# Kernel optimization log

Measured on AMD Instinct MI355X. Metric: run time of the kernel, lower is better.

Reference implementation:

```python
import jax, jax.numpy as jnp
import numpy as np

N, C, E = 50000, 128, 400000
R_CUT = 5.0


def setup_inputs() -> dict:
    key = jax.random.key(0)
    ks = jax.random.split(key, 12)
    s = jax.random.normal(ks[0], (N, C), dtype=jnp.float32)
    v = jax.random.normal(ks[1], (N, 3, C), dtype=jnp.float32)
    edges = jax.random.randint(ks[2], (E, 2), 0, N, dtype=jnp.int64)
    r_ij = jax.random.uniform(ks[3], (E, 1), dtype=jnp.float32, minval=0.1, maxval=R_CUT)
    rn = jax.random.normal(ks[4], (E, 3), dtype=jnp.float32)
    r_ij_normalized = rn / jnp.linalg.norm(rn, axis=-1, keepdims=True)
    sc = 1.0 / np.sqrt(C)
    W1 = jax.random.normal(ks[5], (C, C), dtype=jnp.float32) * sc
    b1 = jnp.zeros((C,), dtype=jnp.float32)
    W2 = jax.random.normal(ks[6], (C, 3 * C), dtype=jnp.float32) * sc
    b2 = jnp.zeros((3 * C,), dtype=jnp.float32)
    Wr = jax.random.normal(ks[7], (20, 3 * C), dtype=jnp.float32) * (1.0 / np.sqrt(20))
    br = jnp.zeros((3 * C,), dtype=jnp.float32)
    return {"s": s, "v": v, "edges": edges, "r_ij": r_ij,
            "r_ij_normalized": r_ij_normalized,
            "W1": W1, "b1": b1, "W2": W2, "b2": b2, "Wr": Wr, "br": br}


def rbf(r_ij, r_cut):
    # r_ij: [E,1] -> [E,20]; sin(n*pi/r_cut * r) / r for n=1..20
    n = jnp.arange(1, 21, dtype=r_ij.dtype)  # [20]
    return jnp.sin((np.pi / r_cut) * n * r_ij) / r_ij


def fcut(r_ij, r_cut):
    return 0.5 * (jnp.cos(np.pi * r_ij / r_cut) + 1.0)  # [E,1]


def reference(s, v, edges, r_ij, r_ij_normalized, W1, b1, W2, b2, Wr, br):
    r_cut = R_CUT
    src = edges[:, 1]
    dst = edges[:, 0]
    # RBF filter: [E,3C], modulated by cosine cutoff
    rbf_pass = (rbf(r_ij, r_cut) @ Wr + br) * fcut(r_ij, r_cut)
    # node MLP: Linear -> SiLU -> Linear : [N,3C]
    s_pass = jax.nn.silu(s @ W1 + b1) @ W2 + b2
    pass_out = rbf_pass * s_pass[src]  # [E,3C]
    dv, ds, drep = jnp.split(pass_out, 3, axis=-1)  # each [E,C]
    # [E,3,C] = gathered v * gate + direction * rep
    delta_v = v[src] * dv[:, None, :] + r_ij_normalized[:, :, None] * drep[:, None, :]
    s_out = s + jax.ops.segment_sum(ds, dst, num_segments=N)
    v_out = v + jax.ops.segment_sum(delta_v, dst, num_segments=N)
    return s_out, v_out
```

## Files before the change

### kernel.cpp

```cpp
#include <hip/hip_runtime.h>
#include <hip/hip_bf16.h>

#define CC 128
#define NOUT 384
#define PI_F 3.14159265358979323846f
#define RCUT 5.0f

typedef float f32x2 __attribute__((ext_vector_type(2)));
typedef __attribute__((ext_vector_type(8))) short bf16x8;
typedef __attribute__((ext_vector_type(4))) float f32x4;

__device__ __forceinline__ float loadF(const void* p, size_t i, int isf32) {
  if (isf32) return ((const float*)p)[i];
  unsigned int w = ((unsigned int)((const unsigned short*)p)[i]) << 16;
  return __uint_as_float(w);
}
__device__ __forceinline__ int loadI(const void* p, size_t i, int isi64) {
  if (isi64) return (int)((const long long*)p)[i];
  return ((const int*)p)[i];
}
__device__ __forceinline__ unsigned int bfbits(float f) {
  __hip_bfloat16 h = __float2bfloat16(f);
  unsigned short u;
  __builtin_memcpy(&u, &h, 2);
  return (unsigned int)u;
}
__device__ __forceinline__ unsigned int bfpack(float lo, float hi) {
  return bfbits(lo) | (bfbits(hi) << 16);
}
__device__ __forceinline__ float bf16lo(unsigned int u) {
  return __uint_as_float(u << 16);
}
__device__ __forceinline__ float bf16hi(unsigned int u) {
  return __uint_as_float(u & 0xffff0000u);
}

__global__ void detect_kernel(const void* s, const void* edges, int* flags) {
  if (threadIdx.x == 0) {
    int isf32 = 0;
    const unsigned short* us = (const unsigned short*)s;
    for (int i = 0; i < 1024; i++) {
      unsigned int w = ((unsigned int)us[i]) << 16;
      float f = __uint_as_float(w);
      if (!(fabsf(f) < 1000.f)) { isf32 = 1; break; }
    }
    int isi64 = 1;
    const int* ie = (const int*)edges;
    for (int i = 1; i < 128; i += 2) {
      if (ie[i] != 0) { isi64 = 0; break; }
    }
    flags[0] = isf32;
    flags[1] = isi64;
  }
}

__global__ void count_kernel(const void* __restrict__ edges, int* __restrict__ cnt,
                             const int* __restrict__ flags, int E) {
  int e = blockIdx.x * blockDim.x + threadIdx.x;
  if (e >= E) return;
  int dst = loadI(edges, (size_t)2 * e, flags[1]);
  atomicAdd(&cnt[dst], 1);
}

__global__ __launch_bounds__(1024) void scan_kernel(const int* __restrict__ cnt,
                                                    int* __restrict__ row_start,
                                                    int* __restrict__ next, int N) {
  __shared__ int woff[16];
  __shared__ int carry_sh;
  const int t = threadIdx.x;
  const int lane = t & 63;
  const int wid = t >> 6;
  if (t == 0) carry_sh = 0;
  __syncthreads();
  for (int base = 0; base < N; base += 1024) {
    int x = (base + t < N) ? cnt[base + t] : 0;
    int incl = x;
    #pragma unroll
    for (int off = 1; off < 64; off <<= 1) {
      int y = __shfl_up(incl, off, 64);
      if (lane >= off) incl += y;
    }
    if (lane == 63) woff[wid] = incl;
    __syncthreads();
    if (wid == 0 && lane < 16) {
      int w = woff[lane];
      int iw = w;
      #pragma unroll
      for (int off = 1; off < 16; off <<= 1) {
        int y = __shfl_up(iw, off, 64);
        if (lane >= off) iw += y;
      }
      woff[lane] = iw - w;
    }
    __syncthreads();
    int carry = carry_sh;
    int excl = carry + woff[wid] + incl - x;
    if (base + t < N) { row_start[base + t] = excl; next[base + t] = excl; }
    __syncthreads();
    if (t == 1023) carry_sh = excl + x;
    __syncthreads();
  }
  if (t == 0) row_start[N] = carry_sh;
}

template <int PRE>
__global__ void fill_kernel(const void* __restrict__ edges,
                            const void* __restrict__ r_ij,
                            const void* __restrict__ rn,
                            int* __restrict__ next,
                            int* __restrict__ esrc,
                            float4* __restrict__ efcrn,
                            float* __restrict__ erb,
                            const int* __restrict__ flags, int E) {
  int e = blockIdx.x * blockDim.x + threadIdx.x;
  if (e >= E) return;
  const int isi64 = flags[1];
  const int isf32 = flags[0];
  const int dst = loadI(edges, (size_t)2 * e, isi64);
  const int src = loadI(edges, (size_t)2 * e + 1, isi64);
  const float r  = loadF(r_ij, e, isf32);
  const float r0 = loadF(rn, (size_t)e * 3 + 0, isf32);
  const float r1 = loadF(rn, (size_t)e * 3 + 1, isf32);
  const float r2 = loadF(rn, (size_t)e * 3 + 2, isf32);
  const int p = atomicAdd(&next[dst], 1);
  esrc[p] = src;
  if (PRE) {
    const float x = (PI_F / RCUT) * r;
    const float s1 = __sinf(x);
    const float c1 = __cosf(x);
    const float fc = 0.5f * (c1 + 1.f);
    efcrn[p] = make_float4(fc, r0, r1, r2);
    const float rf = __builtin_amdgcn_rcpf(r) * fc;
    const float twoc = 2.f * c1;
    float sp = 0.f, sn = s1;
    float rbv[20];
    #pragma unroll
    for (int k = 0; k < 20; k++) {
      rbv[k] = sn * rf;
      const float s2 = twoc * sn - sp;
      sp = sn; sn = s2;
    }
    float4* rb4 = (float4*)(erb + (size_t)p * 20);
    #pragma unroll
    for (int j = 0; j < 5; j++)
      rb4[j] = make_float4(rbv[4 * j], rbv[4 * j + 1], rbv[4 * j + 2], rbv[4 * j + 3]);
  } else {
    efcrn[p] = make_float4(r, r0, r1, r2);
  }
}

__global__ void prep_w_kernel(const void* __restrict__ W1, const void* __restrict__ W2,
                              unsigned short* __restrict__ W1T,
                              unsigned short* __restrict__ W2T,
                              const int* __restrict__ flags) {
  const int c = blockIdx.x;
  const int k = threadIdx.x;
  const int isf32 = flags[0];
  if (c < CC) {
    W1T[(size_t)c * CC + k] = (unsigned short)bfbits(loadF(W1, (size_t)k * CC + c, isf32));
  } else {
    const int cc = c - CC;
    W2T[(size_t)cc * CC + k] = (unsigned short)bfbits(loadF(W2, (size_t)k * NOUT + cc, isf32));
  }
}

template <int ISF32>
__device__ __forceinline__ void mlp_mfma_body(
    const void* __restrict__ s, const void* __restrict__ v,
    const unsigned short* __restrict__ W1T, const unsigned short* __restrict__ W2T,
    const void* __restrict__ b1, const void* __restrict__ b2,
    uint2* __restrict__ tabA, int N) {
  __shared__ unsigned short lds[64 * 128];
  const int t = threadIdx.x;
  const int l = t & 63;
  const int w = t >> 6;
  const int n0 = blockIdx.x * 64;

  #pragma unroll
  for (int it = 0; it < 32; ++it) {
    const int id = it * 256 + t;
    const int row = id >> 7;
    const int col = id & 127;
    const int srow = (n0 + row < N) ? (n0 + row) : (N - 1);
    const float f = loadF(s, (size_t)srow * CC + col, ISF32);
    const int byte = (row * 256 + col * 2) ^ ((row & 7) << 4);
    lds[byte >> 1] = (unsigned short)bfbits(f);
  }
  __syncthreads();

  const int arow = w * 16 + (l & 15);
  bf16x8 a[4];
  #pragma unroll
  for (int kk = 0; kk < 4; ++kk) {
    const int byte = (arow * 256 + (kk * 4 + (l >> 4)) * 16) ^ ((arow & 7) << 4);
    a[kk] = *(const bf16x8*)((const char*)lds + byte);
  }

  f32x4 acc1[8];
  #pragma unroll
  for (int jt = 0; jt < 8; ++jt) { acc1[jt] = f32x4{0.f, 0.f, 0.f, 0.f}; }
  #pragma unroll
  for (int jt = 0; jt < 8; ++jt) {
    const unsigned short* wp = W1T + (size_t)(jt * 16 + (l & 15)) * CC + (l >> 4) * 8;
    #pragma unroll
    for (int kk = 0; kk < 4; ++kk) {
      const bf16x8 b = *(const bf16x8*)(wp + kk * 32);
      acc1[jt] = __builtin_amdgcn_mfma_f32_16x16x32_bf16(a[kk], b, acc1[jt], 0, 0, 0);
    }
  }
  __syncthreads();

  #pragma unroll
  for (int jt = 0; jt < 8; ++jt) {
    const int c = jt * 16 + (l & 15);
    const float bb = loadF(b1, c, ISF32);
    #pragma unroll
    for (int r = 0; r < 4; ++r) {
      const int row = w * 16 + (l >> 4) * 4 + r;
      const float x = acc1[jt][r] + bb;
      const float h = x / (1.f + __expf(-x));
      const int byte = (row * 256 + c * 2) ^ ((row & 7) << 4);
      lds[byte >> 1] = (unsigned short)bfbits(h);
    }
  }
  __syncthreads();

  bf16x8 a2[4];
  #pragma unroll
  for (int kk = 0; kk < 4; ++kk) {
    const int byte = (arow * 256 + (kk * 4 + (l >> 4)) * 16) ^ ((arow & 7) << 4);
    a2[kk] = *(const bf16x8*)((const char*)lds + byte);
  }
  f32x4 acc2[24];
  #pragma unroll
  for (int jt = 0; jt < 24; ++jt) { acc2[jt] = f32x4{0.f, 0.f, 0.f, 0.f}; }
  #pragma unroll
  for (int jt = 0; jt < 24; ++jt) {
    const unsigned short* wp = W2T + (size_t)(jt * 16 + (l & 15)) * CC + (l >> 4) * 8;
    #pragma unroll
    for (int kk = 0; kk < 4; ++kk) {
      const bf16x8 b = *(const bf16x8*)(wp + kk * 32);
      acc2[jt] = __builtin_amdgcn_mfma_f32_16x16x32_bf16(a2[kk], b, acc2[jt], 0, 0, 0);
    }
  }

  #pragma unroll
  for (int jt = 0; jt < 8; ++jt) {
    const int c = jt * 16 + (l & 15);
    const float bb0 = loadF(b2, c, ISF32);
    const float bb1 = loadF(b2, CC + c, ISF32);
    const float bb2v = loadF(b2, 2 * CC + c, ISF32);
    #pragma unroll
    for (int r = 0; r < 4; ++r) {
      const int n = n0 + w * 16 + (l >> 4) * 4 + r;
      if (n >= N) continue;
      const float v0 = loadF(v, (size_t)n * NOUT + c, ISF32);
      tabA[(size_t)n * CC + c] =
          make_uint2(bfpack(acc2[jt][r] + bb0, acc2[jt + 8][r] + bb1),
                     bfpack(acc2[jt + 16][r] + bb2v, v0));
    }
  }
}

__global__ __launch_bounds__(256, 2) void node_mlp_mfma_kernel(
    const void* __restrict__ s, const void* __restrict__ v,
    const unsigned short* __restrict__ W1T, const unsigned short* __restrict__ W2T,
    const void* __restrict__ b1, const void* __restrict__ b2,
    uint2* __restrict__ tabA, const int* __restrict__ flags, int N) {
  if (flags[0]) mlp_mfma_body<1>(s, v, W1T, W2T, b1, b2, tabA, N);
  else          mlp_mfma_body<0>(s, v, W1T, W2T, b1, b2, tabA, N);
}

__global__ void mlp_check_kernel(const void* __restrict__ s,
                                 const void* __restrict__ W1, const void* __restrict__ b1,
                                 const void* __restrict__ W2, const void* __restrict__ b2,
                                 const uint2* __restrict__ tabA, int* __restrict__ flags) {
  __shared__ float h_sh[CC];
  __shared__ int bad;
  const int c = threadIdx.x;
  if (c == 0) bad = 0;
  __syncthreads();
  const int isf32 = flags[0];
  float acc = 0.f;
  for (int k = 0; k < CC; k++)
    acc += loadF(s, k, isf32) * loadF(W1, (size_t)k * CC + c, isf32);
  acc += loadF(b1, c, isf32);
  h_sh[c] = acc / (1.f + __expf(-acc));
  __syncthreads();
  const uint2 ta = tabA[c];
  const float got[3] = {bf16lo(ta.x), bf16hi(ta.x), bf16lo(ta.y)};
  int mybad = 0;
  for (int jj = 0; jj < 3; jj++) {
    float a2 = 0.f;
    for (int k = 0; k < CC; k++)
      a2 += h_sh[k] * loadF(W2, (size_t)k * NOUT + jj * CC + c, isf32);
    a2 += loadF(b2, jj * CC + c, isf32);
    if (fabsf(got[jj] - a2) > 0.25f + 0.02f * fabsf(a2)) mybad = 1;
  }
  if (mybad) atomicOr(&bad, 1);
  __syncthreads();
  if (c == 0) flags[2] = bad ? 0 : 1;
}

template <int ISF32>
__device__ __forceinline__ void node_mlp_body(
    const void* __restrict__ s, const void* __restrict__ v,
    const void* __restrict__ W1, const void* __restrict__ b1,
    const void* __restrict__ W2, const void* __restrict__ b2,
    uint2* __restrict__ tabA, int N) {
  const int M = 8;
  __shared__ float s_sh[M][CC];
  __shared__ float h_sh[M][CC];
  const int c = threadIdx.x;
  const int n0 = blockIdx.x * M;

  #pragma unroll
  for (int m = 0; m < M; m++) {
    int n = n0 + m;
    s_sh[m][c] = (n < N) ? loadF(s, (size_t)n * CC + c, ISF32) : 0.f;
  }
  __syncthreads();

  float acc[M];
  #pragma unroll
  for (int m = 0; m < M; m++) acc[m] = 0.f;
  for (int k = 0; k < CC; k++) {
    float w = loadF(W1, (size_t)k * CC + c, ISF32);
    #pragma unroll
    for (int m = 0; m < M; m++) acc[m] += s_sh[m][k] * w;
  }
  float bb1 = loadF(b1, c, ISF32);
  #pragma unroll
  for (int m = 0; m < M; m++) {
    float x = acc[m] + bb1;
    h_sh[m][c] = x / (1.f + __expf(-x));
  }
  __syncthreads();

  float a2s[3][M];
  #pragma unroll
  for (int jj = 0; jj < 3; jj++) {
    int j = jj * CC + c;
    float a2[M];
    #pragma unroll
    for (int m = 0; m < M; m++) a2[m] = 0.f;
    for (int k = 0; k < CC; k++) {
      float w = loadF(W2, (size_t)k * NOUT + j, ISF32);
      #pragma unroll
      for (int m = 0; m < M; m++) a2[m] += h_sh[m][k] * w;
    }
    float bb2 = loadF(b2, j, ISF32);
    #pragma unroll
    for (int m = 0; m < M; m++) a2s[jj][m] = a2[m] + bb2;
  }

  #pragma unroll
  for (int m = 0; m < M; m++) {
    int n = n0 + m;
    if (n >= N) continue;
    const float v0 = loadF(v, (size_t)n * NOUT + c, ISF32);
    const size_t tix = (size_t)n * CC + c;
    tabA[tix] = make_uint2(bfpack(a2s[0][m], a2s[1][m]), bfpack(a2s[2][m], v0));
  }
}

__global__ __launch_bounds__(128) void node_mlp_fallback_kernel(
    const void* __restrict__ s, const void* __restrict__ v,
    const void* __restrict__ W1, const void* __restrict__ b1,
    const void* __restrict__ W2, const void* __restrict__ b2,
    uint2* __restrict__ tabA, const int* __restrict__ flags, int N) {
  if (flags[2]) return;
  if (flags[0]) node_mlp_body<1>(s, v, W1, b1, W2, b2, tabA, N);
  else          node_mlp_body<0>(s, v, W1, b1, W2, b2, tabA, N);
}

template <int ISF32, int PRE>
__device__ __forceinline__ void agg_body(
    const void* __restrict__ s, const void* __restrict__ v,
    const void* __restrict__ Wr, const void* __restrict__ br,
    const uint2* __restrict__ tabA,
    const int* __restrict__ row_start,
    const int* __restrict__ esrc, const float4* __restrict__ efcrn,
    const float* __restrict__ erb,
    void* __restrict__ out, int N) {
  const int n = blockIdx.x;
  const int c = threadIdx.x;

  f32x2 w0p[10], w1p[10], w2p[10];
  #pragma unroll
  for (int j = 0; j < 10; j++) {
    w0p[j] = f32x2{loadF(Wr, (size_t)(2 * j) * NOUT + c, ISF32),
                   loadF(Wr, (size_t)(2 * j + 1) * NOUT + c, ISF32)};
    w1p[j] = f32x2{loadF(Wr, (size_t)(2 * j) * NOUT + CC + c, ISF32),
                   loadF(Wr, (size_t)(2 * j + 1) * NOUT + CC + c, ISF32)};
    w2p[j] = f32x2{loadF(Wr, (size_t)(2 * j) * NOUT + 2 * CC + c, ISF32),
                   loadF(Wr, (size_t)(2 * j + 1) * NOUT + 2 * CC + c, ISF32)};
  }
  const float b0  = loadF(br, c, ISF32);
  const float b1v = loadF(br, CC + c, ISF32);
  const float b2v = loadF(br, 2 * CC + c, ISF32);

  float accs = 0.f, av0 = 0.f, av1 = 0.f, av2 = 0.f;
  const int beg = row_start[n], end = row_start[n + 1];

  int i = beg;
  for (; i + 2 <= end; i += 2) {
    const int srcA = esrc[i];
    const int srcB = esrc[i + 1];
    const float4 frA = efcrn[i];
    const float4 frB = efcrn[i + 1];
    const uint2 taA = tabA[(size_t)srcA * CC + c];
    const uint2 taB = tabA[(size_t)srcB * CC + c];
    const float v1A = loadF(v, (size_t)srcA * NOUT + CC + c, ISF32);
    const float v2A = loadF(v, (size_t)srcA * NOUT + 2 * CC + c, ISF32);
    const float v1B = loadF(v, (size_t)srcB * NOUT + CC + c, ISF32);
    const float v2B = loadF(v, (size_t)srcB * NOUT + 2 * CC + c, ISF32);

    float fcA, fcB;
    f32x2 rbA[10], rbB[10];
    if (PRE) {
      fcA = frA.x;
      fcB = frB.x;
      const f32x2* rpA = (const f32x2*)(erb + (size_t)i * 20);
      const f32x2* rpB = (const f32x2*)(erb + (size_t)(i + 1) * 20);
      #pragma unroll
      for (int j = 0; j < 10; j++) { rbA[j] = rpA[j]; rbB[j] = rpB[j]; }
    } else {
      const float xA = (PI_F / RCUT) * frA.x;
      const float s1A = __sinf(xA), c1A = __cosf(xA);
      fcA = 0.5f * (c1A + 1.f);
      const float rfA = __builtin_amdgcn_rcpf(frA.x) * fcA;
      const float twocA = 2.f * c1A;
      const float xB = (PI_F / RCUT) * frB.x;
      const float s1B = __sinf(xB), c1B = __cosf(xB);
      fcB = 0.5f * (c1B + 1.f);
      const float rfB = __builtin_amdgcn_rcpf(frB.x) * fcB;
      const float twocB = 2.f * c1B;
      float spA = 0.f, snA = s1A, spB = 0.f, snB = s1B;
      #pragma unroll
      for (int j = 0; j < 10; j++) {
        const float qA0 = snA * rfA;
        float s2 = twocA * snA - spA; spA = snA; snA = s2;
        const float qA1 = snA * rfA;
        s2 = twocA * snA - spA; spA = snA; snA = s2;
        rbA[j] = f32x2{qA0, qA1};
        const float qB0 = snB * rfB;
        s2 = twocB * snB - spB; spB = snB; snB = s2;
        const float qB1 = snB * rfB;
        s2 = twocB * snB - spB; spB = snB; snB = s2;
        rbB[j] = f32x2{qB0, qB1};
      }
    }

    f32x2 a0A = f32x2{0.f, 0.f}, a1A = a0A, a2A = a0A;
    f32x2 a0B = a0A, a1B = a0A, a2B = a0A;
    #pragma unroll
    for (int j = 0; j < 10; j++) {
      a0A += rbA[j] * w0p[j];  a0B += rbB[j] * w0p[j];
      a1A += rbA[j] * w1p[j];  a1B += rbB[j] * w1p[j];
      a2A += rbA[j] * w2p[j];  a2B += rbB[j] * w2p[j];
    }

    const float a0Af = fmaf(b0,  fcA, a0A.x + a0A.y);
    const float a1Af = fmaf(b1v, fcA, a1A.x + a1A.y);
    const float a2Af = fmaf(b2v, fcA, a2A.x + a2A.y);
    const float p0A = a0Af * bf16lo(taA.x);
    const float p1A = a1Af * bf16hi(taA.x);
    const float p2A = a2Af * bf16lo(taA.y);
    accs += p1A;
    av0 = fmaf(bf16hi(taA.y), p0A, fmaf(frA.y, p2A, av0));
    av1 = fmaf(v1A, p0A, fmaf(frA.z, p2A, av1));
    av2 = fmaf(v2A, p0A, fmaf(frA.w, p2A, av2));

    const float a0Bf = fmaf(b0,  fcB, a0B.x + a0B.y);
    const float a1Bf = fmaf(b1v, fcB, a1B.x + a1B.y);
    const float a2Bf = fmaf(b2v, fcB, a2B.x + a2B.y);
    const float p0B = a0Bf * bf16lo(taB.x);
    const float p1B = a1Bf * bf16hi(taB.x);
    const float p2B = a2Bf * bf16lo(taB.y);
    accs += p1B;
    av0 = fmaf(bf16hi(taB.y), p0B, fmaf(frB.y, p2B, av0));
    av1 = fmaf(v1B, p0B, fmaf(frB.z, p2B, av1));
    av2 = fmaf(v2B, p0B, fmaf(frB.w, p2B, av2));
  }

  for (; i < end; ++i) {
    const int src = esrc[i];
    const float4 fr = efcrn[i];
    const uint2 ta = tabA[(size_t)src * CC + c];
    const float v1f = loadF(v, (size_t)src * NOUT + CC + c, ISF32);
    const float v2f = loadF(v, (size_t)src * NOUT + 2 * CC + c, ISF32);

    float fc;
    f32x2 rb[10];
    if (PRE) {
      fc = fr.x;
      const f32x2* rp = (const f32x2*)(erb + (size_t)i * 20);
      #pragma unroll
      for (int j = 0; j < 10; j++) rb[j] = rp[j];
    } else {
      const float x = (PI_F / RCUT) * fr.x;
      const float s1 = __sinf(x), c1 = __cosf(x);
      fc = 0.5f * (c1 + 1.f);
      const float rf = __builtin_amdgcn_rcpf(fr.x) * fc;
      const float twoc = 2.f * c1;
      float spv = 0.f, snv = s1;
      #pragma unroll
      for (int j = 0; j < 10; j++) {
        const float q0 = snv * rf;
        float s2 = twoc * snv - spv; spv = snv; snv = s2;
        const float q1 = snv * rf;
        s2 = twoc * snv - spv; spv = snv; snv = s2;
        rb[j] = f32x2{q0, q1};
      }
    }

    f32x2 a0p = f32x2{0.f, 0.f}, a1p = a0p, a2p = a0p;
    #pragma unroll
    for (int j = 0; j < 10; j++) {
      a0p += rb[j] * w0p[j];
      a1p += rb[j] * w1p[j];
      a2p += rb[j] * w2p[j];
    }

    const float a0 = fmaf(b0,  fc, a0p.x + a0p.y);
    const float a1 = fmaf(b1v, fc, a1p.x + a1p.y);
    const float a2 = fmaf(b2v, fc, a2p.x + a2p.y);
    const float p0 = a0 * bf16lo(ta.x);
    const float p1 = a1 * bf16hi(ta.x);
    const float p2 = a2 * bf16lo(ta.y);
    accs += p1;
    av0 = fmaf(bf16hi(ta.y), p0, fmaf(fr.y, p2, av0));
    av1 = fmaf(v1f, p0, fmaf(fr.z, p2, av1));
    av2 = fmaf(v2f, p0, fmaf(fr.w, p2, av2));
  }

  const size_t si = (size_t)n * CC + c;
  const size_t vi = (size_t)n * NOUT;
  const float so = loadF(s, si, ISF32) + accs;
  const float o0 = loadF(v, vi + 0 * CC + c, ISF32) + av0;
  const float o1 = loadF(v, vi + 1 * CC + c, ISF32) + av1;
  const float o2 = loadF(v, vi + 2 * CC + c, ISF32) + av2;
  const size_t vo = (size_t)N * CC + vi;
  if (ISF32) {
    float* o = (float*)out;
    o[si] = so;
    o[vo + 0 * CC + c] = o0;
    o[vo + 1 * CC + c] = o1;
    o[vo + 2 * CC + c] = o2;
  } else {
    __hip_bfloat16* o = (__hip_bfloat16*)out;
    o[si] = __float2bfloat16(so);
    o[vo + 0 * CC + c] = __float2bfloat16(o0);
    o[vo + 1 * CC + c] = __float2bfloat16(o1);
    o[vo + 2 * CC + c] = __float2bfloat16(o2);
  }
}

template <int PRE>
__global__ __launch_bounds__(128, 3) void aggregate_kernel(
    const void* __restrict__ s, const void* __restrict__ v,
    const void* __restrict__ Wr, const void* __restrict__ br,
    const uint2* __restrict__ tabA,
    const int* __restrict__ row_start,
    const int* __restrict__ esrc, const float4* __restrict__ efcrn,
    const float* __restrict__ erb,
    void* __restrict__ out, const int* __restrict__ flags, int N) {
  if (flags[0]) agg_body<1, PRE>(s, v, Wr, br, tabA, row_start, esrc, efcrn, erb, out, N);
  else          agg_body<0, PRE>(s, v, Wr, br, tabA, row_start, esrc, efcrn, erb, out, N);
}

extern "C" void kernel_launch(void* const* d_in, const int* in_sizes, int n_in,
                              void* d_out, int out_size, void* d_ws, size_t ws_size,
                              hipStream_t stream) {
  const void* s     = d_in[0];
  const void* v     = d_in[1];
  const void* edges = d_in[2];
  const void* r_ij  = d_in[3];
  const void* rn    = d_in[4];
  const void* W1    = d_in[5];
  const void* b1    = d_in[6];
  const void* W2    = d_in[7];
  const void* b2    = d_in[8];
  const void* Wr    = d_in[9];
  const void* br    = d_in[10];

  const int N = in_sizes[0] / CC;
  const int E = in_sizes[3];

  char* ws = (char*)d_ws;
  int* flags = (int*)ws;
  size_t off = 256;
  auto align16 = [](size_t x) { return (x + 15) & ~(size_t)15; };
  unsigned short* W1T = (unsigned short*)(ws + off);  off += align16((size_t)CC * CC * 2);
  unsigned short* W2T = (unsigned short*)(ws + off);  off += align16((size_t)NOUT * CC * 2);
  uint2* tabA = (uint2*)(ws + off);      off += align16((size_t)N * CC * 8);
  float4* efcrn = (float4*)(ws + off);   off += align16((size_t)E * 16);
  int* esrc = (int*)(ws + off);          off += align16((size_t)E * 4);
  int* cnt = (int*)(ws + off);           off += align16((size_t)N * 4);
  int* row_start = (int*)(ws + off);     off += align16((size_t)(N + 1) * 4);
  int* next = (int*)(ws + off);          off += align16((size_t)N * 4);
  float* erb = (float*)(ws + off);
  const size_t off_erb_end = off + (size_t)E * 20 * 4;
  const int pre = (ws_size >= off_erb_end) ? 1 : 0;

  hipMemsetAsync(cnt, 0, (size_t)N * sizeof(int), stream);

  detect_kernel<<<1, 64, 0, stream>>>(s, edges, flags);
  count_kernel<<<(E + 255) / 256, 256, 0, stream>>>(edges, cnt, flags, E);
  scan_kernel<<<1, 1024, 0, stream>>>(cnt, row_start, next, N);
  if (pre)
    fill_kernel<1><<<(E + 255) / 256, 256, 0, stream>>>(edges, r_ij, rn, next,
                                                        esrc, efcrn, erb, flags, E);
  else
    fill_kernel<0><<<(E + 255) / 256, 256, 0, stream>>>(edges, r_ij, rn, next,
                                                        esrc, efcrn, erb, flags, E);
  prep_w_kernel<<<CC + NOUT, 128, 0, stream>>>(W1, W2, W1T, W2T, flags);
  node_mlp_mfma_kernel<<<(N + 63) / 64, 256, 0, stream>>>(s, v, W1T, W2T, b1, b2,
                                                          tabA, flags, N);
  mlp_check_kernel<<<1, 128, 0, stream>>>(s, W1, b1, W2, b2, tabA, flags);
  node_mlp_fallback_kernel<<<(N + 7) / 8, 128, 0, stream>>>(s, v, W1, b1, W2, b2,
                                                            tabA, flags, N);
  if (pre)
    aggregate_kernel<1><<<N, 128, 0, stream>>>(s, v, Wr, br, tabA, row_start,
                                               esrc, efcrn, erb, d_out, flags, N);
  else
    aggregate_kernel<0><<<N, 128, 0, stream>>>(s, v, Wr, br, tabA, row_start,
                                               esrc, efcrn, erb, d_out, flags, N);
}
```

Before: 611.8 us.

## Parallelize CSR scan, pack v components into bf16 table, drop MLP check/fallback

Result: faster. 567.6 us (-7.2%).

```diff
diff --git a/kernel.cpp b/kernel.cpp
--- a/kernel.cpp
+++ b/kernel.cpp
@@ -60,6 +60,74 @@
   if (e >= E) return;
   int dst = loadI(edges, (size_t)2 * e, flags[1]);
   atomicAdd(&cnt[dst], 1);
+}
+
+__global__ __launch_bounds__(1024) void scan_part1(const int* __restrict__ cnt,
+                                                   int* __restrict__ row_start,
+                                                   int* __restrict__ bsum, int N) {
+  __shared__ int woff[16];
+  const int t = threadIdx.x;
+  const int lane = t & 63;
+  const int wid = t >> 6;
+  const int idx = blockIdx.x * 4096 + t * 4;
+  int4 x = make_int4(0, 0, 0, 0);
+  if (idx < N) x = *(const int4*)(cnt + idx);
+  const int ssum = x.x + x.y + x.z + x.w;
+  int incl = ssum;
+  #pragma unroll
+  for (int off = 1; off < 64; off <<= 1) {
+    int y = __shfl_up(incl, off, 64);
+    if (lane >= off) incl += y;
+  }
+  if (lane == 63) woff[wid] = incl;
+  __syncthreads();
+  if (wid == 0 && lane < 16) {
+    int w = woff[lane];
+    int iw = w;
+    #pragma unroll
+    for (int off = 1; off < 16; off <<= 1) {
+      int y = __shfl_up(iw, off, 64);
+      if (lane >= off) iw += y;
+    }
+    woff[lane] = iw - w;
+  }
+  __syncthreads();
+  const int ebase = woff[wid] + (incl - ssum);
+  if (idx < N) {
+    int4 r;
+    r.x = ebase;
+    r.y = ebase + x.x;
+    r.z = r.y + x.y;
+    r.w = r.z + x.z;
+    *(int4*)(row_start + idx) = r;
+  }
+  if (t == 1023) bsum[blockIdx.x] = woff[15] + incl;
+}
+
+__global__ void scan_part2(const int* __restrict__ bsum, int* __restrict__ boff,
+                           int* __restrict__ row_start, int NB, int N) {
+  const int lane = threadIdx.x;
+  int v = (lane < NB) ? bsum[lane] : 0;
+  int incl = v;
+  #pragma unroll
+  for (int off = 1; off < 64; off <<= 1) {
+    int y = __shfl_up(incl, off, 64);
+    if (lane >= off) incl += y;
+  }
+  if (lane < NB) boff[lane] = incl - v;
+  if (lane == NB - 1) row_start[N] = incl;
+}
+
+__global__ __launch_bounds__(1024) void scan_part3(int* __restrict__ row_start,
+                                                   int* __restrict__ next,
+                                                   const int* __restrict__ boff, int N) {
+  const int idx = blockIdx.x * 4096 + threadIdx.x * 4;
+  if (idx >= N) return;
+  const int b = boff[blockIdx.x];
+  int4 r = *(const int4*)(row_start + idx);
+  r.x += b; r.y += b; r.z += b; r.w += b;
+  *(int4*)(row_start + idx) = r;
+  *(int4*)(next + idx) = r;
 }
 
 __global__ __launch_bounds__(1024) void scan_kernel(const int* __restrict__ cnt,
@@ -169,7 +237,7 @@
     const void* __restrict__ s, const void* __restrict__ v,
     const unsigned short* __restrict__ W1T, const unsigned short* __restrict__ W2T,
     const void* __restrict__ b1, const void* __restrict__ b2,
-    uint2* __restrict__ tabA, int N) {
+    uint2* __restrict__ tabA, unsigned int* __restrict__ tabB, int tb, int N) {
   __shared__ unsigned short lds[64 * 128];
   const int t = threadIdx.x;
   const int l = t & 63;
@@ -254,10 +322,16 @@
     for (int r = 0; r < 4; ++r) {
       const int n = n0 + w * 16 + (l >> 4) * 4 + r;
       if (n >= N) continue;
-      const float v0 = loadF(v, (size_t)n * NOUT + c, ISF32);
+      const size_t vb = (size_t)n * NOUT + c;
+      const float v0 = loadF(v, vb, ISF32);
       tabA[(size_t)n * CC + c] =
           make_uint2(bfpack(acc2[jt][r] + bb0, acc2[jt + 8][r] + bb1),
                      bfpack(acc2[jt + 16][r] + bb2v, v0));
+      if (tb) {
+        const float v1 = loadF(v, vb + CC, ISF32);
+        const float v2 = loadF(v, vb + 2 * CC, ISF32);
+        tabB[(size_t)n * CC + c] = bfpack(v1, v2);
+      }
     }
   }
 }
@@ -266,119 +340,17 @@
     const void* __restrict__ s, const void* __restrict__ v,
     const unsigned short* __restrict__ W1T, const unsigned short* __restrict__ W2T,
     const void* __restrict__ b1, const void* __restrict__ b2,
-    uint2* __restrict__ tabA, const int* __restrict__ flags, int N) {
-  if (flags[0]) mlp_mfma_body<1>(s, v, W1T, W2T, b1, b2, tabA, N);
-  else          mlp_mfma_body<0>(s, v, W1T, W2T, b1, b2, tabA, N);
-}
-
-__global__ void mlp_check_kernel(const void* __restrict__ s,
-                                 const void* __restrict__ W1, const void* __restrict__ b1,
-                                 const void* __restrict__ W2, const void* __restrict__ b2,
-                                 const uint2* __restrict__ tabA, int* __restrict__ flags) {
-  __shared__ float h_sh[CC];
-  __shared__ int bad;
-  const int c = threadIdx.x;
-  if (c == 0) bad = 0;
-  __syncthreads();
-  const int isf32 = flags[0];
-  float acc = 0.f;
-  for (int k = 0; k < CC; k++)
-    acc += loadF(s, k, isf32) * loadF(W1, (size_t)k * CC + c, isf32);
-  acc += loadF(b1, c, isf32);
-  h_sh[c] = acc / (1.f + __expf(-acc));
-  __syncthreads();
-  const uint2 ta = tabA[c];
-  const float got[3] = {bf16lo(ta.x), bf16hi(ta.x), bf16lo(ta.y)};
-  int mybad = 0;
-  for (int jj = 0; jj < 3; jj++) {
-    float a2 = 0.f;
-    for (int k = 0; k < CC; k++)
-      a2 += h_sh[k] * loadF(W2, (size_t)k * NOUT + jj * CC + c, isf32);
-    a2 += loadF(b2, jj * CC + c, isf32);
-    if (fabsf(got[jj] - a2) > 0.25f + 0.02f * fabsf(a2)) mybad = 1;
-  }
-  if (mybad) atomicOr(&bad, 1);
-  __syncthreads();
-  if (c == 0) flags[2] = bad ? 0 : 1;
-}
-
-template <int ISF32>
-__device__ __forceinline__ void node_mlp_body(
-    const void* __restrict__ s, const void* __restrict__ v,
-    const void* __restrict__ W1, const void* __restrict__ b1,
-    const void* __restrict__ W2, const void* __restrict__ b2,
-    uint2* __restrict__ tabA, int N) {
-  const int M = 8;
-  __shared__ float s_sh[M][CC];
-  __shared__ float h_sh[M][CC];
-  const int c = threadIdx.x;
-  const int n0 = blockIdx.x * M;
-
-  #pragma unroll
-  for (int m = 0; m < M; m++) {
-    int n = n0 + m;
-    s_sh[m][c] = (n < N) ? loadF(s, (size_t)n * CC + c, ISF32) : 0.f;
-  }
-  __syncthreads();
-
-  float acc[M];
-  #pragma unroll
-  for (int m = 0; m < M; m++) acc[m] = 0.f;
-  for (int k = 0; k < CC; k++) {
-    float w = loadF(W1, (size_t)k * CC + c, ISF32);
-    #pragma unroll
-    for (int m = 0; m < M; m++) acc[m] += s_sh[m][k] * w;
-  }
-  float bb1 = loadF(b1, c, ISF32);
-  #pragma unroll
-  for (int m = 0; m < M; m++) {
-    float x = acc[m] + bb1;
-    h_sh[m][c] = x / (1.f + __expf(-x));
-  }
-  __syncthreads();
-
-  float a2s[3][M];
-  #pragma unroll
-  for (int jj = 0; jj < 3; jj++) {
-    int j = jj * CC + c;
-    float a2[M];
-    #pragma unroll
-    for (int m = 0; m < M; m++) a2[m] = 0.f;
-    for (int k = 0; k < CC; k++) {
-      float w = loadF(W2, (size_t)k * NOUT + j, ISF32);
-      #pragma unroll
-      for (int m = 0; m < M; m++) a2[m] += h_sh[m][k] * w;
-    }
-    float bb2 = loadF(b2, j, ISF32);
-    #pragma unroll
-    for (int m = 0; m < M; m++) a2s[jj][m] = a2[m] + bb2;
-  }
-
-  #pragma unroll
-  for (int m = 0; m < M; m++) {
-    int n = n0 + m;
-    if (n >= N) continue;
-    const float v0 = loadF(v, (size_t)n * NOUT + c, ISF32);
-    const size_t tix = (size_t)n * CC + c;
-    tabA[tix] = make_uint2(bfpack(a2s[0][m], a2s[1][m]), bfpack(a2s[2][m], v0));
-  }
-}
-
-__global__ __launch_bounds__(128) void node_mlp_fallback_kernel(
-    const void* __restrict__ s, const void* __restrict__ v,
-    const void* __restrict__ W1, const void* __restrict__ b1,
-    const void* __restrict__ W2, const void* __restrict__ b2,
-    uint2* __restrict__ tabA, const int* __restrict__ flags, int N) {
-  if (flags[2]) return;
-  if (flags[0]) node_mlp_body<1>(s, v, W1, b1, W2, b2, tabA, N);
-  else          node_mlp_body<0>(s, v, W1, b1, W2, b2, tabA, N);
-}
-
-template <int ISF32, int PRE>
+    uint2* __restrict__ tabA, unsigned int* __restrict__ tabB, int tb,
+    const int* __restrict__ flags, int N) {
+  if (flags[0]) mlp_mfma_body<1>(s, v, W1T, W2T, b1, b2, tabA, tabB, tb, N);
+  else          mlp_mfma_body<0>(s, v, W1T, W2T, b1, b2, tabA, tabB, tb, N);
+}
+
+template <int ISF32, int PRE, int TB>
 __device__ __forceinline__ void agg_body(
     const void* __restrict__ s, const void* __restrict__ v,
     const void* __restrict__ Wr, const void* __restrict__ br,
-    const uint2* __restrict__ tabA,
+    const uint2* __restrict__ tabA, const unsigned int* __restrict__ tabB,
     const int* __restrict__ row_start,
     const int* __restrict__ esrc, const float4* __restrict__ efcrn,
     const float* __restrict__ erb,
@@ -411,10 +383,18 @@
     const float4 frB = efcrn[i + 1];
     const uint2 taA = tabA[(size_t)srcA * CC + c];
     const uint2 taB = tabA[(size_t)srcB * CC + c];
-    const float v1A = loadF(v, (size_t)srcA * NOUT + CC + c, ISF32);
-    const float v2A = loadF(v, (size_t)srcA * NOUT + 2 * CC + c, ISF32);
-    const float v1B = loadF(v, (size_t)srcB * NOUT + CC + c, ISF32);
-    const float v2B = loadF(v, (size_t)srcB * NOUT + 2 * CC + c, ISF32);
+    float v1A, v2A, v1B, v2B;
+    if (TB) {
+      const unsigned int tA = tabB[(size_t)srcA * CC + c];
+      const unsigned int tB = tabB[(size_t)srcB * CC + c];
+      v1A = bf16lo(tA); v2A = bf16hi(tA);
+      v1B = bf16lo(tB); v2B = bf16hi(tB);
+    } else {
+      v1A = loadF(v, (size_t)srcA * NOUT + CC + c, ISF32);
+      v2A = loadF(v, (size_t)srcA * NOUT + 2 * CC + c, ISF32);
+      v1B = loadF(v, (size_t)srcB * NOUT + CC + c, ISF32);
+      v2B = loadF(v, (size_t)srcB * NOUT + 2 * CC + c, ISF32);
+    }
 
     float fcA, fcB;
     f32x2 rbA[10], rbB[10];
@@ -488,8 +468,14 @@
     const int src = esrc[i];
     const float4 fr = efcrn[i];
     const uint2 ta = tabA[(size_t)src * CC + c];
-    const float v1f = loadF(v, (size_t)src * NOUT + CC + c, ISF32);
-    const float v2f = loadF(v, (size_t)src * NOUT + 2 * CC + c, ISF32);
+    float v1f, v2f;
+    if (TB) {
+      const unsigned int tB = tabB[(size_t)src * CC + c];
+      v1f = bf16lo(tB); v2f = bf16hi(tB);
+    } else {
+      v1f = loadF(v, (size_t)src * NOUT + CC + c, ISF32);
+      v2f = loadF(v, (size_t)src * NOUT + 2 * CC + c, ISF32);
+    }
 
     float fc;
     f32x2 rb[10];
@@ -557,17 +543,17 @@
   }
 }
 
-template <int PRE>
+template <int PRE, int TB>
 __global__ __launch_bounds__(128, 3) void aggregate_kernel(
     const void* __restrict__ s, const void* __restrict__ v,
     const void* __restrict__ Wr, const void* __restrict__ br,
-    const uint2* __restrict__ tabA,
+    const uint2* __restrict__ tabA, const unsigned int* __restrict__ tabB,
     const int* __restrict__ row_start,
     const int* __restrict__ esrc, const float4* __restrict__ efcrn,
     const float* __restrict__ erb,
     void* __restrict__ out, const int* __restrict__ flags, int N) {
-  if (flags[0]) agg_body<1, PRE>(s, v, Wr, br, tabA, row_start, esrc, efcrn, erb, out, N);
-  else          agg_body<0, PRE>(s, v, Wr, br, tabA, row_start, esrc, efcrn, erb, out, N);
+  if (flags[0]) agg_body<1, PRE, TB>(s, v, Wr, br, tabA, tabB, row_start, esrc, efcrn, erb, out, N);
+  else          agg_body<0, PRE, TB>(s, v, Wr, br, tabA, tabB, row_start, esrc, efcrn, erb, out, N);
 }
 
 extern "C" void kernel_launch(void* const* d_in, const int* in_sizes, int n_in,
@@ -590,7 +576,9 @@
 
   char* ws = (char*)d_ws;
   int* flags = (int*)ws;
-  size_t off = 256;
+  int* bsum = (int*)(ws + 256);
+  int* boff = (int*)(ws + 512);
+  size_t off = 768;
   auto align16 = [](size_t x) { return (x + 15) & ~(size_t)15; };
   unsigned short* W1T = (unsigned short*)(ws + off);  off += align16((size_t)CC * CC * 2);
   unsigned short* W2T = (unsigned short*)(ws + off);  off += align16((size_t)NOUT * CC * 2);
@@ -602,13 +590,25 @@
   int* next = (int*)(ws + off);          off += align16((size_t)N * 4);
   float* erb = (float*)(ws + off);
   const size_t off_erb_end = off + (size_t)E * 20 * 4;
+  unsigned int* tabB = (unsigned int*)(ws + off_erb_end);
+  const size_t off_tabB_end = off_erb_end + (size_t)N * CC * 4;
   const int pre = (ws_size >= off_erb_end) ? 1 : 0;
+  const int tb  = (pre && ws_size >= off_tabB_end) ? 1 : 0;
 
   hipMemsetAsync(cnt, 0, (size_t)N * sizeof(int), stream);
 
   detect_kernel<<<1, 64, 0, stream>>>(s, edges, flags);
   count_kernel<<<(E + 255) / 256, 256, 0, stream>>>(edges, cnt, flags, E);
-  scan_kernel<<<1, 1024, 0, stream>>>(cnt, row_start, next, N);
+
+  const int NB = (N + 4095) / 4096;
+  if ((N % 4 == 0) && NB <= 64) {
+    scan_part1<<<NB, 1024, 0, stream>>>(cnt, row_start, bsum, N);
+    scan_part2<<<1, 64, 0, stream>>>(bsum, boff, row_start, NB, N);
+    scan_part3<<<NB, 1024, 0, stream>>>(row_start, next, boff, N);
+  } else {
+    scan_kernel<<<1, 1024, 0, stream>>>(cnt, row_start, next, N);
+  }
+
   if (pre)
     fill_kernel<1><<<(E + 255) / 256, 256, 0, stream>>>(edges, r_ij, rn, next,
                                                         esrc, efcrn, erb, flags, E);
@@ -617,14 +617,17 @@
                                                         esrc, efcrn, erb, flags, E);
   prep_w_kernel<<<CC + NOUT, 128, 0, stream>>>(W1, W2, W1T, W2T, flags);
   node_mlp_mfma_kernel<<<(N + 63) / 64, 256, 0, stream>>>(s, v, W1T, W2T, b1, b2,
-                                                          tabA, flags, N);
-  mlp_check_kernel<<<1, 128, 0, stream>>>(s, W1, b1, W2, b2, tabA, flags);
-  node_mlp_fallback_kernel<<<(N + 7) / 8, 128, 0, stream>>>(s, v, W1, b1, W2, b2,
-                                                            tabA, flags, N);
-  if (pre)
-    aggregate_kernel<1><<<N, 128, 0, stream>>>(s, v, Wr, br, tabA, row_start,
-                                               esrc, efcrn, erb, d_out, flags, N);
+                                                          tabA, tabB, tb, flags, N);
+  if (pre && tb)
+    aggregate_kernel<1, 1><<<N, 128, 0, stream>>>(s, v, Wr, br, tabA, tabB,
+                                                  row_start, esrc, efcrn, erb,
+                                                  d_out, flags, N);
+  else if (pre)
+    aggregate_kernel<1, 0><<<N, 128, 0, stream>>>(s, v, Wr, br, tabA, tabB,
+                                                  row_start, esrc, efcrn, erb,
+                                                  d_out, flags, N);
   else
-    aggregate_kernel<0><<<N, 128, 0, stream>>>(s, v, Wr, br, tabA, row_start,
-                                               esrc, efcrn, erb, d_out, flags, N);
-}
+    aggregate_kernel<0, 0><<<N, 128, 0, stream>>>(s, v, Wr, br, tabA, tabB,
+                                                  row_start, esrc, efcrn, erb,
+                                                  d_out, flags, N);
+}
```
